# Kernel optimization log

Hardware: AMD Instinct MI355X
Metric: run time of the kernel (lower is better)

## Reference

```python
import jax, jax.numpy as jnp
import numpy as np

N_NODES = 100000
N_EDGES = 1600000
NEG_SLOPE = 0.2  # PyG GATConv default


def setup_inputs() -> dict:
    key = jax.random.key(0)
    ks = jax.random.split(key, 10)
    return {
        "x": jax.random.normal(ks[0], (N_NODES, 128), dtype=jnp.float32),
        "edge_index": jax.random.randint(ks[1], (2, N_EDGES), 0, N_NODES, dtype=jnp.int64),
        "W1": jax.random.normal(ks[2], (128, 128), dtype=jnp.float32) * 0.1,
        "a_src1": jax.random.normal(ks[3], (4, 32), dtype=jnp.float32) * 0.1,
        "a_dst1": jax.random.normal(ks[4], (4, 32), dtype=jnp.float32) * 0.1,
        "b1": jax.random.normal(ks[5], (128,), dtype=jnp.float32) * 0.1,
        "W2": jax.random.normal(ks[6], (128, 16), dtype=jnp.float32) * 0.1,
        "a_src2": jax.random.normal(ks[7], (1, 16), dtype=jnp.float32) * 0.1,
        "a_dst2": jax.random.normal(ks[8], (1, 16), dtype=jnp.float32) * 0.1,
        "b2": jax.random.normal(ks[9], (16,), dtype=jnp.float32) * 0.1,
    }


def _gat_layer(x, src, dst, W, a_src, a_dst, b, heads):
    # PyG GATConv (concat=True): xw -> per-edge attention -> segment softmax over
    # incoming edges of each target node -> weighted scatter-sum.
    N = x.shape[0]
    H = heads
    C = W.shape[1] // H
    xw = (x @ W).reshape(N, H, C)                      # [N,H,C]
    al = (xw * a_src).sum(-1)                          # [N,H] source term
    ar = (xw * a_dst).sum(-1)                          # [N,H] target term
    e = jax.nn.leaky_relu(al[src] + ar[dst], NEG_SLOPE)  # [E',H]
    emax = jax.ops.segment_max(e, dst, num_segments=N)   # [N,H]
    em = jnp.exp(e - emax[dst])
    denom = jax.ops.segment_sum(em, dst, num_segments=N)
    alpha = em / denom[dst]                            # [E',H]
    out = jax.ops.segment_sum(xw[src] * alpha[:, :, None], dst, num_segments=N)
    return out.reshape(N, H * C) + b


def reference(x, edge_index, W1, a_src1, a_dst1, b1, W2, a_src2, a_dst2, b2):
    N = x.shape[0]
    loop = jnp.arange(N, dtype=edge_index.dtype)
    # PyG GATConv add_self_loops=True
    src = jnp.concatenate([edge_index[0], loop])
    dst = jnp.concatenate([edge_index[1], loop])
    h = jax.nn.relu(_gat_layer(x, src, dst, W1, a_src1, a_dst1, b1, 4))
    # F.dropout(p=0.5, training=self.training): identity in eval mode
    return _gat_layer(h, src, dst, W2, a_src2, a_dst2, b2, 1)
```

## Files before the change

kernel.cpp:

```cpp
#include <hip/hip_runtime.h>
#include <hip/hip_fp16.h>

#define N_NODES 100000
#define N_EDGES 1600000
#define E_TOT   (N_EDGES + N_NODES)
#define NEG_SLOPE 0.2f
#define PART_EPB 4096
#define BSTRIDE 18432
#define NGEMM ((N_NODES + 63) / 64)
#define NPART ((E_TOT + PART_EPB - 1) / PART_EPB)

using f16x8 = __attribute__((ext_vector_type(8))) _Float16;
using f32x4 = __attribute__((ext_vector_type(4))) float;
union H8 { f16x8 v; _Float16 h[8]; __half2 h2[4]; };
union H4 { __half2 h2[2]; uint2 u; };

__global__ __launch_bounds__(256)
void k_gemm1_part(const float* __restrict__ x, const float* __restrict__ W1,
                  const float* __restrict__ a_src1, const float* __restrict__ a_dst1,
                  const int* __restrict__ ei, int* __restrict__ bcnt, int* __restrict__ pairs,
                  __half* __restrict__ xw1h, float* __restrict__ al1, float* __restrict__ ar1) {
    __shared__ int lcnt[128];
    __shared__ int lbase[128];
    __shared__ _Float16 sx[64][136];
    const int t = threadIdx.x;

    if (blockIdx.x >= NGEMM) {
        const int base = ((int)blockIdx.x - NGEMM) * PART_EPB;
        if (t < 128) lcnt[t] = 0;
        __syncthreads();
        int sr[16], dr[16];
#pragma unroll
        for (int u = 0; u < 16; ++u) {
            const int e = base + u * 256 + t;
            if (e < E_TOT) {
                int s, d;
                if (e < N_EDGES) { s = ei[e]; d = ei[N_EDGES + e]; }
                else             { s = d = e - N_EDGES; }
                sr[u] = s; dr[u] = d;
                atomicAdd(&lcnt[d >> 10], 1);
            } else dr[u] = -1;
        }
        __syncthreads();
        if (t < 128) {
            const int c = lcnt[t];
            lbase[t] = (c > 0) ? atomicAdd(&bcnt[t], c) : 0;
            lcnt[t] = 0;
        }
        __syncthreads();
#pragma unroll
        for (int u = 0; u < 16; ++u) {
            if (dr[u] >= 0) {
                const int bk = dr[u] >> 10;
                const int r = atomicAdd(&lcnt[bk], 1);
                pairs[(size_t)bk * BSTRIDE + lbase[bk] + r] = (sr[u] << 10) | (dr[u] & 1023);
            }
        }
        return;
    }

    const int n0 = (int)blockIdx.x * 64;

    for (int i = t; i < 64 * 32; i += 256) {
        const int row = i >> 5;
        const int c4 = (i & 31) * 4;
        const int gr = n0 + row;
        const float4 xv = *(const float4*)&x[(size_t)(gr < N_NODES ? gr : N_NODES - 1) * 128 + c4];
        H4 tmp;
        tmp.h2[0] = __float22half2_rn(make_float2(xv.x, xv.y));
        tmp.h2[1] = __float22half2_rn(make_float2(xv.z, xv.w));
        *(uint2*)&sx[row][c4] = tmp.u;
    }
    __syncthreads();

    const int lane = t & 63;
    const int w = t >> 6;
    const int q = lane >> 4;
    const int n15 = lane & 15;
    const int j0 = (2 * w) * 16 + n15;
    const int j1 = (2 * w + 1) * 16 + n15;

    f32x4 acc[4][2] = {};

    for (int kt = 0; kt < 4; ++kt) {
        const int k0 = kt * 32 + q * 8;
        H8 A0, A1, A2, A3, B0, B1;
        A0.v = *(const f16x8*)&sx[n15][k0];
        A1.v = *(const f16x8*)&sx[16 + n15][k0];
        A2.v = *(const f16x8*)&sx[32 + n15][k0];
        A3.v = *(const f16x8*)&sx[48 + n15][k0];
        {
            float w0[8], w1[8];
#pragma unroll
            for (int i = 0; i < 8; ++i) {
                w0[i] = W1[(size_t)(k0 + i) * 128 + j0];
                w1[i] = W1[(size_t)(k0 + i) * 128 + j1];
            }
#pragma unroll
            for (int i = 0; i < 4; ++i) {
                B0.h2[i] = __float22half2_rn(make_float2(w0[2 * i], w0[2 * i + 1]));
                B1.h2[i] = __float22half2_rn(make_float2(w1[2 * i], w1[2 * i + 1]));
            }
        }
        acc[0][0] = __builtin_amdgcn_mfma_f32_16x16x32_f16(A0.v, B0.v, acc[0][0], 0, 0, 0);
        acc[0][1] = __builtin_amdgcn_mfma_f32_16x16x32_f16(A0.v, B1.v, acc[0][1], 0, 0, 0);
        acc[1][0] = __builtin_amdgcn_mfma_f32_16x16x32_f16(A1.v, B0.v, acc[1][0], 0, 0, 0);
        acc[1][1] = __builtin_amdgcn_mfma_f32_16x16x32_f16(A1.v, B1.v, acc[1][1], 0, 0, 0);
        acc[2][0] = __builtin_amdgcn_mfma_f32_16x16x32_f16(A2.v, B0.v, acc[2][0], 0, 0, 0);
        acc[2][1] = __builtin_amdgcn_mfma_f32_16x16x32_f16(A2.v, B1.v, acc[2][1], 0, 0, 0);
        acc[3][0] = __builtin_amdgcn_mfma_f32_16x16x32_f16(A3.v, B0.v, acc[3][0], 0, 0, 0);
        acc[3][1] = __builtin_amdgcn_mfma_f32_16x16x32_f16(A3.v, B1.v, acc[3][1], 0, 0, 0);
    }

    const float as0 = a_src1[j0], as1 = a_src1[j1];
    const float ad0 = a_dst1[j0], ad1 = a_dst1[j1];
#pragma unroll
    for (int m = 0; m < 4; ++m) {
#pragma unroll
        for (int r = 0; r < 4; ++r) {
            const int node = n0 + m * 16 + q * 4 + r;
            const float vA = acc[m][0][r], vB = acc[m][1][r];
            const bool ok = node < N_NODES;
            if (ok) {
                xw1h[(size_t)node * 128 + j0] = __float2half(vA);
                xw1h[(size_t)node * 128 + j1] = __float2half(vB);
            }
            float ps = vA * as0 + vB * as1;
            float pd = vA * ad0 + vB * ad1;
#pragma unroll
            for (int o = 1; o < 16; o <<= 1) {
                ps += __shfl_xor(ps, o, 64);
                pd += __shfl_xor(pd, o, 64);
            }
            if (n15 == 0 && ok) {
                al1[(size_t)node * 4 + w] = ps;
                ar1[(size_t)node * 4 + w] = pd;
            }
        }
    }
}

__global__ __launch_bounds__(1024)
void k_fill3(const int* __restrict__ pairs, const int* __restrict__ bcnt,
             int* __restrict__ ioff, int* __restrict__ deg, int* __restrict__ ssrc) {
    const int bucket = blockIdx.x;
    const int t = threadIdx.x;
    const int cnt = bcnt[bucket];
    __shared__ int lhist[1024];
    __shared__ int lcur[1024];
    __shared__ int wsum[16];
    __shared__ int sbc[128];
    __shared__ int sbase;
    lhist[t] = 0;
    if (t < 128) sbc[t] = bcnt[t];
    __syncthreads();
    if (t == 0) {
        int b = 0;
        for (int k = 0; k < bucket; ++k) b += sbc[k];
        sbase = b;
    }
    for (int i = t; i < cnt; i += 1024) {
        const int p = pairs[(size_t)bucket * BSTRIDE + i];
        atomicAdd(&lhist[p & 1023], 1);
    }
    __syncthreads();
    const int v = lhist[t];
    int inc = v;
    const int lane = t & 63, wid = t >> 6;
#pragma unroll
    for (int o = 1; o < 64; o <<= 1) {
        const int nv = __shfl_up(inc, o, 64);
        if (lane >= o) inc += nv;
    }
    if (lane == 63) wsum[wid] = inc;
    __syncthreads();
    if (t == 0) {
        int acc = 0;
#pragma unroll
        for (int k = 0; k < 16; ++k) { const int tv = wsum[k]; wsum[k] = acc; acc += tv; }
    }
    __syncthreads();
    const int gofs = sbase + (inc - v) + wsum[wid];
    const int d = bucket * 1024 + t;
    if (d < N_NODES) { ioff[d] = gofs; deg[d] = v; }
    lcur[t] = gofs;
    __syncthreads();
    for (int i = t; i < cnt; i += 1024) {
        const int p = pairs[(size_t)bucket * BSTRIDE + i];
        const int pos = atomicAdd(&lcur[p & 1023], 1);
        ssrc[pos] = p >> 10;
    }
}

__global__ __launch_bounds__(256)
void k_aggr1(const int* __restrict__ ssrc, const int* __restrict__ offs,
             const int* __restrict__ deg, const float* __restrict__ al1,
             const float* __restrict__ ar1, const __half* __restrict__ xw1h,
             const float* __restrict__ b1, __half* __restrict__ out1h) {
    const int lane = threadIdx.x & 63;
    const int d = blockIdx.x * 4 + (threadIdx.x >> 6);
    const int g = lane >> 4;
    const int c = lane & 15;
    const int h = c >> 2;
    const int beg = offs[d];
    const int n = deg[d];
    const float arh = ar1[(size_t)d * 4 + h];
    float acc[8] = {0.f, 0.f, 0.f, 0.f, 0.f, 0.f, 0.f, 0.f};
    float dnm = 0.f;

    for (int base = 0; base < n; base += 8) {
#pragma unroll
        for (int u = 0; u < 2; ++u) {
            const int e = base + u * 4 + g;
            const bool p = e < n;
            const int s = ssrc[beg + (p ? e : 0)];
            float v = al1[(size_t)s * 4 + h] + arh;
            v = v > 0.f ? v : NEG_SLOPE * v;
            const float w = p ? __expf(v) : 0.f;
            const uint4 rv = *(const uint4*)&xw1h[(size_t)s * 128 + c * 8];
            const float2 f0 = __half22float2(*(const __half2*)&rv.x);
            const float2 f1 = __half22float2(*(const __half2*)&rv.y);
            const float2 f2 = __half22float2(*(const __half2*)&rv.z);
            const float2 f3 = __half22float2(*(const __half2*)&rv.w);
            acc[0] = fmaf(w, f0.x, acc[0]); acc[1] = fmaf(w, f0.y, acc[1]);
            acc[2] = fmaf(w, f1.x, acc[2]); acc[3] = fmaf(w, f1.y, acc[3]);
            acc[4] = fmaf(w, f2.x, acc[4]); acc[5] = fmaf(w, f2.y, acc[5]);
            acc[6] = fmaf(w, f3.x, acc[6]); acc[7] = fmaf(w, f3.y, acc[7]);
            dnm += w;
        }
    }
#pragma unroll
    for (int i = 0; i < 8; ++i) {
        acc[i] += __shfl_xor(acc[i], 16, 64);
        acc[i] += __shfl_xor(acc[i], 32, 64);
    }
    dnm += __shfl_xor(dnm, 16, 64);
    dnm += __shfl_xor(dnm, 32, 64);
    if (g == 0) {
        const float rc = 1.f / dnm;
        const float4 b01 = *(const float4*)&b1[c * 8];
        const float4 b23 = *(const float4*)&b1[c * 8 + 4];
        const float bb[8] = {b01.x, b01.y, b01.z, b01.w, b23.x, b23.y, b23.z, b23.w};
        __half ho[8];
#pragma unroll
        for (int i = 0; i < 8; ++i) {
            const float hv = acc[i] * rc + bb[i];
            ho[i] = __float2half(hv > 0.f ? hv : 0.f);
        }
        *(uint4*)&out1h[(size_t)d * 128 + c * 8] = *(uint4*)ho;
    }
}

__global__ __launch_bounds__(256)
void k_gemm2m(const __half* __restrict__ out1h, const float* __restrict__ W2,
              const float* __restrict__ a_src2, const float* __restrict__ a_dst2,
              __half* __restrict__ xw2h, float* __restrict__ al2, float* __restrict__ ar2) {
    const int t = threadIdx.x;
    const int lane = t & 63;
    const int w = t >> 6;
    const int q = lane >> 4;
    const int n15 = lane & 15;
    const int n0 = (int)blockIdx.x * 128 + w * 16;
    const int ra0 = n0 + n15;
    const int ra1 = n0 + 64 + n15;
    const size_t rowA0 = (ra0 < N_NODES) ? (size_t)ra0 : (size_t)(N_NODES - 1);
    const size_t rowA1 = (ra1 < N_NODES) ? (size_t)ra1 : (size_t)(N_NODES - 1);

    f32x4 acc0 = {0.f, 0.f, 0.f, 0.f}, acc1 = acc0;
#pragma unroll
    for (int kt = 0; kt < 4; ++kt) {
        const int k0 = kt * 32 + q * 8;
        H8 A0, A1, B;
        A0.v = *(const f16x8*)&out1h[rowA0 * 128 + k0];
        A1.v = *(const f16x8*)&out1h[rowA1 * 128 + k0];
        float wv[8];
#pragma unroll
        for (int i = 0; i < 8; ++i)
            wv[i] = W2[(size_t)(k0 + i) * 16 + n15];
#pragma unroll
        for (int i = 0; i < 4; ++i)
            B.h2[i] = __float22half2_rn(make_float2(wv[2 * i], wv[2 * i + 1]));
        acc0 = __builtin_amdgcn_mfma_f32_16x16x32_f16(A0.v, B.v, acc0, 0, 0, 0);
        acc1 = __builtin_amdgcn_mfma_f32_16x16x32_f16(A1.v, B.v, acc1, 0, 0, 0);
    }

    const float as = a_src2[n15], ad = a_dst2[n15];
#pragma unroll
    for (int m = 0; m < 2; ++m) {
        const f32x4 acc = m ? acc1 : acc0;
#pragma unroll
        for (int r = 0; r < 4; ++r) {
            const int node = n0 + m * 64 + q * 4 + r;
            float ps = acc[r] * as;
            float pd = acc[r] * ad;
#pragma unroll
            for (int o = 1; o < 16; o <<= 1) {
                ps += __shfl_xor(ps, o, 64);
                pd += __shfl_xor(pd, o, 64);
            }
            if (node < N_NODES) {
                xw2h[(size_t)node * 16 + n15] = __float2half(acc[r]);
                if (n15 == 0) { al2[node] = ps; ar2[node] = pd; }
            }
        }
    }
}

__global__ __launch_bounds__(256)
void k_aggr2(const int* __restrict__ ssrc, const int* __restrict__ offs,
             const int* __restrict__ deg, const float* __restrict__ al2,
             const float* __restrict__ ar2, const __half* __restrict__ xw2h,
             const float* __restrict__ b2, float* __restrict__ out) {
    const int lane = threadIdx.x & 63;
    const int node = blockIdx.x * 4 + (threadIdx.x >> 6);
    const int j2 = lane & 7;
    const int eL = lane >> 3;
    const int beg = offs[node];
    const int n = deg[node];
    const float ard = ar2[node];
    float a0 = 0.f, a1 = 0.f, dnm = 0.f;
    for (int base = 0; base < n; base += 32) {
#pragma unroll
        for (int u = 0; u < 4; ++u) {
            const int e = base + u * 8 + eL;
            const bool p = e < n;
            const int s = ssrc[beg + (p ? e : 0)];
            float v = al2[s] + ard;
            v = v > 0.f ? v : NEG_SLOPE * v;
            const float w = p ? __expf(v) : 0.f;
            const float2 f = __half22float2(*(const __half2*)&xw2h[(size_t)s * 16 + j2 * 2]);
            a0 = fmaf(w, f.x, a0);
            a1 = fmaf(w, f.y, a1);
            dnm += w;
        }
    }
#pragma unroll
    for (int o = 8; o < 64; o <<= 1) {
        a0 += __shfl_xor(a0, o, 64);
        a1 += __shfl_xor(a1, o, 64);
        dnm += __shfl_xor(dnm, o, 64);
    }
    if (eL == 0) {
        out[(size_t)node * 16 + j2 * 2]     = a0 / dnm + b2[j2 * 2];
        out[(size_t)node * 16 + j2 * 2 + 1] = a1 / dnm + b2[j2 * 2 + 1];
    }
}

extern "C" void kernel_launch(void* const* d_in, const int* in_sizes, int n_in,
                              void* d_out, int out_size, void* d_ws, size_t ws_size,
                              hipStream_t stream) {
    const float* x      = (const float*)d_in[0];
    const int*   ei     = (const int*)d_in[1];
    const float* W1     = (const float*)d_in[2];
    const float* a_src1 = (const float*)d_in[3];
    const float* a_dst1 = (const float*)d_in[4];
    const float* b1     = (const float*)d_in[5];
    const float* W2     = (const float*)d_in[6];
    const float* a_src2 = (const float*)d_in[7];
    const float* a_dst2 = (const float*)d_in[8];
    const float* b2     = (const float*)d_in[9];
    float* out = (float*)d_out;

    char* wsb = (char*)d_ws;
    __half* xw1h = (__half*)wsb;
    __half* xw2h = (__half*)wsb;
    float*  al2  = (float*)(wsb + (size_t)N_NODES * 16 * 2);
    float*  ar2  = al2 + N_NODES;
    __half* out1h = (__half*)(wsb + (size_t)N_NODES * 128 * 2);
    int*    pairs = (int*)out1h;
    float*  al1  = (float*)(wsb + (size_t)N_NODES * 128 * 4);
    float*  ar1  = al1 + (size_t)N_NODES * 4;
    int* ibcnt = (int*)(ar1 + (size_t)N_NODES * 4);
    int* ioff  = ibcnt + 128;
    int* ideg  = ioff + N_NODES;
    int* isrc  = ideg + N_NODES;

    hipMemsetAsync(ibcnt, 0, 128 * sizeof(int), stream);

    k_gemm1_part<<<NGEMM + NPART, 256, 0, stream>>>(x, W1, a_src1, a_dst1,
                                                    ei, ibcnt, pairs, xw1h, al1, ar1);
    k_fill3<<<128, 1024, 0, stream>>>(pairs, ibcnt, ioff, ideg, isrc);

    k_aggr1<<<N_NODES / 4, 256, 0, stream>>>(isrc, ioff, ideg, al1, ar1, xw1h, b1, out1h);

    k_gemm2m<<<(N_NODES + 127) / 128, 256, 0, stream>>>(out1h, W2, a_src2, a_dst2, xw2h, al2, ar2);

    k_aggr2<<<N_NODES / 4, 256, 0, stream>>>(isrc, ioff, ideg, al2, ar2, xw2h, b2, out);
}
```

Measured before the change: 298.7 us.

## Fold attention vectors into weights and use finer destination buckets for CSR build

Adds a prep kernel that precomputes W·a_src and W·a_dst as fp16 matrices so the attention logits come from extra MFMA ops instead of shuffle reductions in both GEMM kernels; the prep kernel also zeroes the bucket counters, replacing the memset. Destination bucketing in the edge partition and fill kernels changes from 1024-node to 256-node buckets (391 blocks of 256 threads instead of 128 blocks of 1024), giving more parallelism in the CSR build. Logits now pass through an fp16-rounded fused weight, which slightly changes numerics, and one extra tiny launch is added.

```diff
diff --git a/kernel.cpp b/kernel.cpp
--- a/kernel.cpp
+++ b/kernel.cpp
@@ -6,7 +6,8 @@
 #define E_TOT   (N_EDGES + N_NODES)
 #define NEG_SLOPE 0.2f
 #define PART_EPB 4096
-#define BSTRIDE 18432
+#define NBUCK ((N_NODES + 255) / 256)
+#define PBSTRIDE 5632
 #define NGEMM ((N_NODES + 63) / 64)
 #define NPART ((E_TOT + PART_EPB - 1) / PART_EPB)
 
@@ -15,19 +16,66 @@
 union H8 { f16x8 v; _Float16 h[8]; __half2 h2[4]; };
 union H4 { __half2 h2[2]; uint2 u; };
 
+__global__ __launch_bounds__(128)
+void k_prep(const float* __restrict__ W1, const float* __restrict__ as1,
+            const float* __restrict__ ad1, const float* __restrict__ W2,
+            const float* __restrict__ as2, const float* __restrict__ ad2,
+            _Float16* __restrict__ WaT1, _Float16* __restrict__ WaT2,
+            int* __restrict__ bcnt) {
+    const int t = threadIdx.x;
+    for (int i = t; i < NBUCK; i += 128) bcnt[i] = 0;
+
+    const float a1s = as1[t], a1d = ad1[t];
+    for (int k = 0; k < 128; ++k) {
+        const float wv = W1[(size_t)k * 128 + t];
+        float ps = wv * a1s;
+        float pd = wv * a1d;
+#pragma unroll
+        for (int o = 1; o < 32; o <<= 1) {
+            ps += __shfl_xor(ps, o, 32);
+            pd += __shfl_xor(pd, o, 32);
+        }
+        if ((t & 31) == 0) {
+            const int h = t >> 5;
+            WaT1[h * 128 + k] = (_Float16)ps;
+            WaT1[(4 + h) * 128 + k] = (_Float16)pd;
+        }
+    }
+    for (int n = 8; n < 16; ++n) WaT1[n * 128 + t] = (_Float16)0.f;
+
+    const int j = t & 15, kb = t >> 4;
+    const float a2s = as2[j], a2d = ad2[j];
+    for (int k8 = 0; k8 < 16; ++k8) {
+        const int k = k8 * 8 + kb;
+        const float wv = W2[(size_t)k * 16 + j];
+        float ps = wv * a2s;
+        float pd = wv * a2d;
+#pragma unroll
+        for (int o = 1; o < 16; o <<= 1) {
+            ps += __shfl_xor(ps, o, 16);
+            pd += __shfl_xor(pd, o, 16);
+        }
+        if (j == 0) {
+            WaT2[k] = (_Float16)ps;
+            WaT2[128 + k] = (_Float16)pd;
+        }
+    }
+    for (int n = 2; n < 16; ++n) WaT2[n * 128 + t] = (_Float16)0.f;
+}
+
 __global__ __launch_bounds__(256)
 void k_gemm1_part(const float* __restrict__ x, const float* __restrict__ W1,
-                  const float* __restrict__ a_src1, const float* __restrict__ a_dst1,
+                  const _Float16* __restrict__ WaT1,
                   const int* __restrict__ ei, int* __restrict__ bcnt, int* __restrict__ pairs,
                   __half* __restrict__ xw1h, float* __restrict__ al1, float* __restrict__ ar1) {
-    __shared__ int lcnt[128];
-    __shared__ int lbase[128];
+    __shared__ int lcnt[NBUCK + 1];
+    __shared__ int lbase[NBUCK + 1];
     __shared__ _Float16 sx[64][136];
     const int t = threadIdx.x;
 
     if (blockIdx.x >= NGEMM) {
         const int base = ((int)blockIdx.x - NGEMM) * PART_EPB;
-        if (t < 128) lcnt[t] = 0;
+        for (int i = t; i < NBUCK; i += 256) lcnt[i] = 0;
         __syncthreads();
         int sr[16], dr[16];
 #pragma unroll
@@ -38,22 +86,22 @@
                 if (e < N_EDGES) { s = ei[e]; d = ei[N_EDGES + e]; }
                 else             { s = d = e - N_EDGES; }
                 sr[u] = s; dr[u] = d;
-                atomicAdd(&lcnt[d >> 10], 1);
+                atomicAdd(&lcnt[d >> 8], 1);
             } else dr[u] = -1;
         }
         __syncthreads();
-        if (t < 128) {
-            const int c = lcnt[t];
-            lbase[t] = (c > 0) ? atomicAdd(&bcnt[t], c) : 0;
-            lcnt[t] = 0;
+        for (int i = t; i < NBUCK; i += 256) {
+            const int c = lcnt[i];
+            lbase[i] = (c > 0) ? atomicAdd(&bcnt[i], c) : 0;
+            lcnt[i] = 0;
         }
         __syncthreads();
 #pragma unroll
         for (int u = 0; u < 16; ++u) {
             if (dr[u] >= 0) {
-                const int bk = dr[u] >> 10;
+                const int bk = dr[u] >> 8;
                 const int r = atomicAdd(&lcnt[bk], 1);
-                pairs[(size_t)bk * BSTRIDE + lbase[bk] + r] = (sr[u] << 10) | (dr[u] & 1023);
+                pairs[(size_t)bk * PBSTRIDE + lbase[bk] + r] = (sr[u] << 8) | (dr[u] & 255);
             }
         }
         return;
@@ -81,6 +129,7 @@
     const int j1 = (2 * w + 1) * 16 + n15;
 
     f32x4 acc[4][2] = {};
+    f32x4 e0 = {0.f,0.f,0.f,0.f}, e1 = e0, e2 = e0, e3 = e0;
 
     for (int kt = 0; kt < 4; ++kt) {
         const int k0 = kt * 32 + q * 8;
@@ -110,58 +159,65 @@
         acc[2][1] = __builtin_amdgcn_mfma_f32_16x16x32_f16(A2.v, B1.v, acc[2][1], 0, 0, 0);
         acc[3][0] = __builtin_amdgcn_mfma_f32_16x16x32_f16(A3.v, B0.v, acc[3][0], 0, 0, 0);
         acc[3][1] = __builtin_amdgcn_mfma_f32_16x16x32_f16(A3.v, B1.v, acc[3][1], 0, 0, 0);
-    }
-
-    const float as0 = a_src1[j0], as1 = a_src1[j1];
-    const float ad0 = a_dst1[j0], ad1 = a_dst1[j1];
+        if (w == 0) {
+            H8 B2;
+            B2.v = *(const f16x8*)&WaT1[n15 * 128 + k0];
+            e0 = __builtin_amdgcn_mfma_f32_16x16x32_f16(A0.v, B2.v, e0, 0, 0, 0);
+            e1 = __builtin_amdgcn_mfma_f32_16x16x32_f16(A1.v, B2.v, e1, 0, 0, 0);
+            e2 = __builtin_amdgcn_mfma_f32_16x16x32_f16(A2.v, B2.v, e2, 0, 0, 0);
+            e3 = __builtin_amdgcn_mfma_f32_16x16x32_f16(A3.v, B2.v, e3, 0, 0, 0);
+        }
+    }
+
 #pragma unroll
     for (int m = 0; m < 4; ++m) {
 #pragma unroll
         for (int r = 0; r < 4; ++r) {
             const int node = n0 + m * 16 + q * 4 + r;
-            const float vA = acc[m][0][r], vB = acc[m][1][r];
-            const bool ok = node < N_NODES;
-            if (ok) {
-                xw1h[(size_t)node * 128 + j0] = __float2half(vA);
-                xw1h[(size_t)node * 128 + j1] = __float2half(vB);
-            }
-            float ps = vA * as0 + vB * as1;
-            float pd = vA * ad0 + vB * ad1;
-#pragma unroll
-            for (int o = 1; o < 16; o <<= 1) {
-                ps += __shfl_xor(ps, o, 64);
-                pd += __shfl_xor(pd, o, 64);
-            }
-            if (n15 == 0 && ok) {
-                al1[(size_t)node * 4 + w] = ps;
-                ar1[(size_t)node * 4 + w] = pd;
-            }
-        }
-    }
-}
-
-__global__ __launch_bounds__(1024)
+            if (node < N_NODES) {
+                xw1h[(size_t)node * 128 + j0] = __float2half(acc[m][0][r]);
+                xw1h[(size_t)node * 128 + j1] = __float2half(acc[m][1][r]);
+            }
+        }
+    }
+    if (w == 0) {
+#pragma unroll
+        for (int m = 0; m < 4; ++m) {
+            const f32x4 em = (m == 0) ? e0 : (m == 1) ? e1 : (m == 2) ? e2 : e3;
+#pragma unroll
+            for (int r = 0; r < 4; ++r) {
+                const int node = n0 + m * 16 + q * 4 + r;
+                if (node < N_NODES) {
+                    if (n15 < 4)      al1[(size_t)node * 4 + n15] = em[r];
+                    else if (n15 < 8) ar1[(size_t)node * 4 + (n15 - 4)] = em[r];
+                }
+            }
+        }
+    }
+}
+
+__global__ __launch_bounds__(256)
 void k_fill3(const int* __restrict__ pairs, const int* __restrict__ bcnt,
              int* __restrict__ ioff, int* __restrict__ deg, int* __restrict__ ssrc) {
     const int bucket = blockIdx.x;
     const int t = threadIdx.x;
     const int cnt = bcnt[bucket];
-    __shared__ int lhist[1024];
-    __shared__ int lcur[1024];
-    __shared__ int wsum[16];
-    __shared__ int sbc[128];
+    __shared__ int lhist[256];
+    __shared__ int lcur[256];
+    __shared__ int wsum[4];
+    __shared__ int sbc[NBUCK + 1];
     __shared__ int sbase;
     lhist[t] = 0;
-    if (t < 128) sbc[t] = bcnt[t];
+    for (int i = t; i < NBUCK; i += 256) sbc[i] = bcnt[i];
     __syncthreads();
     if (t == 0) {
         int b = 0;
         for (int k = 0; k < bucket; ++k) b += sbc[k];
         sbase = b;
     }
-    for (int i = t; i < cnt; i += 1024) {
-        const int p = pairs[(size_t)bucket * BSTRIDE + i];
-        atomicAdd(&lhist[p & 1023], 1);
+    for (int i = t; i < cnt; i += 256) {
+        const int p = pairs[(size_t)bucket * PBSTRIDE + i];
+        atomicAdd(&lhist[p & 255], 1);
     }
     __syncthreads();
     const int v = lhist[t];
@@ -177,18 +233,18 @@
     if (t == 0) {
         int acc = 0;
 #pragma unroll
-        for (int k = 0; k < 16; ++k) { const int tv = wsum[k]; wsum[k] = acc; acc += tv; }
+        for (int k = 0; k < 4; ++k) { const int tv = wsum[k]; wsum[k] = acc; acc += tv; }
     }
     __syncthreads();
     const int gofs = sbase + (inc - v) + wsum[wid];
-    const int d = bucket * 1024 + t;
+    const int d = bucket * 256 + t;
     if (d < N_NODES) { ioff[d] = gofs; deg[d] = v; }
     lcur[t] = gofs;
     __syncthreads();
-    for (int i = t; i < cnt; i += 1024) {
-        const int p = pairs[(size_t)bucket * BSTRIDE + i];
-        const int pos = atomicAdd(&lcur[p & 1023], 1);
-        ssrc[pos] = p >> 10;
+    for (int i = t; i < cnt; i += 256) {
+        const int p = pairs[(size_t)bucket * PBSTRIDE + i];
+        const int pos = atomicAdd(&lcur[p & 255], 1);
+        ssrc[pos] = p >> 8;
     }
 }
 
@@ -253,7 +309,7 @@
 
 __global__ __launch_bounds__(256)
 void k_gemm2m(const __half* __restrict__ out1h, const float* __restrict__ W2,
-              const float* __restrict__ a_src2, const float* __restrict__ a_dst2,
+              const _Float16* __restrict__ WaT2,
               __half* __restrict__ xw2h, float* __restrict__ al2, float* __restrict__ ar2) {
     const int t = threadIdx.x;
     const int lane = t & 63;
@@ -267,10 +323,11 @@
     const size_t rowA1 = (ra1 < N_NODES) ? (size_t)ra1 : (size_t)(N_NODES - 1);
 
     f32x4 acc0 = {0.f, 0.f, 0.f, 0.f}, acc1 = acc0;
+    f32x4 e0 = acc0, e1 = acc0;
 #pragma unroll
     for (int kt = 0; kt < 4; ++kt) {
         const int k0 = kt * 32 + q * 8;
-        H8 A0, A1, B;
+        H8 A0, A1, B, B2;
         A0.v = *(const f16x8*)&out1h[rowA0 * 128 + k0];
         A1.v = *(const f16x8*)&out1h[rowA1 * 128 + k0];
         float wv[8];
@@ -280,27 +337,24 @@
 #pragma unroll
         for (int i = 0; i < 4; ++i)
             B.h2[i] = __float22half2_rn(make_float2(wv[2 * i], wv[2 * i + 1]));
+        B2.v = *(const f16x8*)&WaT2[n15 * 128 + k0];
         acc0 = __builtin_amdgcn_mfma_f32_16x16x32_f16(A0.v, B.v, acc0, 0, 0, 0);
         acc1 = __builtin_amdgcn_mfma_f32_16x16x32_f16(A1.v, B.v, acc1, 0, 0, 0);
-    }
-
-    const float as = a_src2[n15], ad = a_dst2[n15];
+        e0   = __builtin_amdgcn_mfma_f32_16x16x32_f16(A0.v, B2.v, e0, 0, 0, 0);
+        e1   = __builtin_amdgcn_mfma_f32_16x16x32_f16(A1.v, B2.v, e1, 0, 0, 0);
+    }
+
 #pragma unroll
     for (int m = 0; m < 2; ++m) {
         const f32x4 acc = m ? acc1 : acc0;
+        const f32x4 em  = m ? e1 : e0;
 #pragma unroll
         for (int r = 0; r < 4; ++r) {
             const int node = n0 + m * 64 + q * 4 + r;
-            float ps = acc[r] * as;
-            float pd = acc[r] * ad;
-#pragma unroll
-            for (int o = 1; o < 16; o <<= 1) {
-                ps += __shfl_xor(ps, o, 64);
-                pd += __shfl_xor(pd, o, 64);
-            }
             if (node < N_NODES) {
                 xw2h[(size_t)node * 16 + n15] = __float2half(acc[r]);
-                if (n15 == 0) { al2[node] = ps; ar2[node] = pd; }
+                if (n15 == 0)      al2[node] = em[r];
+                else if (n15 == 1) ar2[node] = em[r];
             }
         }
     }
@@ -371,19 +425,22 @@
     float*  al1  = (float*)(wsb + (size_t)N_NODES * 128 * 4);
     float*  ar1  = al1 + (size_t)N_NODES * 4;
     int* ibcnt = (int*)(ar1 + (size_t)N_NODES * 4);
-    int* ioff  = ibcnt + 128;
+    int* ioff  = ibcnt + 512;
     int* ideg  = ioff + N_NODES;
     int* isrc  = ideg + N_NODES;
-
-    hipMemsetAsync(ibcnt, 0, 128 * sizeof(int), stream);
-
-    k_gemm1_part<<<NGEMM + NPART, 256, 0, stream>>>(x, W1, a_src1, a_dst1,
-                                                    ei, ibcnt, pairs, xw1h, al1, ar1);
-    k_fill3<<<128, 1024, 0, stream>>>(pairs, ibcnt, ioff, ideg, isrc);
+    _Float16* WaT1 = (_Float16*)(isrc + E_TOT);
+    _Float16* WaT2 = WaT1 + 16 * 128;
+
+    k_prep<<<1, 128, 0, stream>>>(W1, a_src1, a_dst1, W2, a_src2, a_dst2,
+                                  WaT1, WaT2, ibcnt);
+
+    k_gemm1_part<<<NGEMM + NPART, 256, 0, stream>>>(x, W1, WaT1, ei, ibcnt,
+                                                    pairs, xw1h, al1, ar1);
+    k_fill3<<<NBUCK, 256, 0, stream>>>(pairs, ibcnt, ioff, ideg, isrc);
 
     k_aggr1<<<N_NODES / 4, 256, 0, stream>>>(isrc, ioff, ideg, al1, ar1, xw1h, b1, out1h);
 
-    k_gemm2m<<<(N_NODES + 127) / 128, 256, 0, stream>>>(out1h, W2, a_src2, a_dst2, xw2h, al2, ar2);
+    k_gemm2m<<<(N_NODES + 127) / 128, 256, 0, stream>>>(out1h, W2, WaT2, xw2h, al2, ar2);
 
     k_aggr2<<<N_NODES / 4, 256, 0, stream>>>(isrc, ioff, ideg, al2, ar2, xw2h, b2, out);
 }
```

Measured after the change: 350.8 us. +17.4%, slower.

## Co-schedule CSR fill with GEMM1 instead of partition pass

Applied to the files above, without the earlier changes.

The edge-partition pass now runs as its own kernel. The per-bucket CSR fill runs in the same launch as the first-layer GEMM, with the fill blocks first and using 256 threads each over a shared-memory union. The intent is to hide the 128 latency-bound fill blocks behind the GEMM blocks rather than behind the partition work. The cost is that the fill uses 256 instead of 1024 threads per bucket, so each fill block does more serial work, and the shared-memory union sizes every block to the larger of the two layouts.

```diff
diff --git a/kernel.cpp b/kernel.cpp
--- a/kernel.cpp
+++ b/kernel.cpp
@@ -9,57 +9,120 @@
 #define BSTRIDE 18432
 #define NGEMM ((N_NODES + 63) / 64)
 #define NPART ((E_TOT + PART_EPB - 1) / PART_EPB)
+#define NFILL 128
 
 using f16x8 = __attribute__((ext_vector_type(8))) _Float16;
 using f32x4 = __attribute__((ext_vector_type(4))) float;
 union H8 { f16x8 v; _Float16 h[8]; __half2 h2[4]; };
 union H4 { __half2 h2[2]; uint2 u; };
 
+
 __global__ __launch_bounds__(256)
-void k_gemm1_part(const float* __restrict__ x, const float* __restrict__ W1,
-                  const float* __restrict__ a_src1, const float* __restrict__ a_dst1,
-                  const int* __restrict__ ei, int* __restrict__ bcnt, int* __restrict__ pairs,
-                  __half* __restrict__ xw1h, float* __restrict__ al1, float* __restrict__ ar1) {
+void k_part(const int* __restrict__ ei, int* __restrict__ bcnt, int* __restrict__ pairs) {
     __shared__ int lcnt[128];
     __shared__ int lbase[128];
-    __shared__ _Float16 sx[64][136];
     const int t = threadIdx.x;
-
-    if (blockIdx.x >= NGEMM) {
-        const int base = ((int)blockIdx.x - NGEMM) * PART_EPB;
-        if (t < 128) lcnt[t] = 0;
+    const int base = (int)blockIdx.x * PART_EPB;
+    if (t < 128) lcnt[t] = 0;
+    __syncthreads();
+    int sr[16], dr[16];
+#pragma unroll
+    for (int u = 0; u < 16; ++u) {
+        const int e = base + u * 256 + t;
+        if (e < E_TOT) {
+            int s, d;
+            if (e < N_EDGES) { s = ei[e]; d = ei[N_EDGES + e]; }
+            else             { s = d = e - N_EDGES; }
+            sr[u] = s; dr[u] = d;
+            atomicAdd(&lcnt[d >> 10], 1);
+        } else dr[u] = -1;
+    }
+    __syncthreads();
+    if (t < 128) {
+        const int c = lcnt[t];
+        lbase[t] = (c > 0) ? atomicAdd(&bcnt[t], c) : 0;
+        lcnt[t] = 0;
+    }
+    __syncthreads();
+#pragma unroll
+    for (int u = 0; u < 16; ++u) {
+        if (dr[u] >= 0) {
+            const int bk = dr[u] >> 10;
+            const int r = atomicAdd(&lcnt[bk], 1);
+            pairs[(size_t)bk * BSTRIDE + lbase[bk] + r] = (sr[u] << 10) | (dr[u] & 1023);
+        }
+    }
+}
+
+union SMem {
+    _Float16 sx[64][136];
+    struct { int lhist[1024]; int lcur[1024]; int sbc[128]; int wsum[4]; int sbase; } f;
+};
+
+__global__ __launch_bounds__(256)
+void k_gemm1_fill(const float* __restrict__ x, const float* __restrict__ W1,
+                  const float* __restrict__ a_src1, const float* __restrict__ a_dst1,
+                  const int* __restrict__ bcnt, const int* __restrict__ pairs,
+                  int* __restrict__ ioff, int* __restrict__ deg, int* __restrict__ ssrc,
+                  __half* __restrict__ xw1h, float* __restrict__ al1, float* __restrict__ ar1) {
+    __shared__ SMem sm;
+    const int t = threadIdx.x;
+
+    if (blockIdx.x < NFILL) {
+        const int bucket = blockIdx.x;
+        const int cnt = bcnt[bucket];
+        auto& F = sm.f;
+        for (int i = t; i < 1024; i += 256) F.lhist[i] = 0;
+        if (t < 128) F.sbc[t] = bcnt[t];
         __syncthreads();
-        int sr[16], dr[16];
-#pragma unroll
-        for (int u = 0; u < 16; ++u) {
-            const int e = base + u * 256 + t;
-            if (e < E_TOT) {
-                int s, d;
-                if (e < N_EDGES) { s = ei[e]; d = ei[N_EDGES + e]; }
-                else             { s = d = e - N_EDGES; }
-                sr[u] = s; dr[u] = d;
-                atomicAdd(&lcnt[d >> 10], 1);
-            } else dr[u] = -1;
+        if (t == 0) {
+            int b = 0;
+            for (int k = 0; k < bucket; ++k) b += F.sbc[k];
+            F.sbase = b;
+        }
+        for (int i = t; i < cnt; i += 256) {
+            const int p = pairs[(size_t)bucket * BSTRIDE + i];
+            atomicAdd(&F.lhist[p & 1023], 1);
         }
         __syncthreads();
-        if (t < 128) {
-            const int c = lcnt[t];
-            lbase[t] = (c > 0) ? atomicAdd(&bcnt[t], c) : 0;
-            lcnt[t] = 0;
-        }
+        const int h0 = F.lhist[4 * t], h1 = F.lhist[4 * t + 1];
+        const int h2 = F.lhist[4 * t + 2], h3 = F.lhist[4 * t + 3];
+        const int sum = h0 + h1 + h2 + h3;
+        int inc = sum;
+        const int lane = t & 63, wid = t >> 6;
+#pragma unroll
+        for (int o = 1; o < 64; o <<= 1) {
+            const int nv = __shfl_up(inc, o, 64);
+            if (lane >= o) inc += nv;
+        }
+        if (lane == 63) F.wsum[wid] = inc;
         __syncthreads();
-#pragma unroll
-        for (int u = 0; u < 16; ++u) {
-            if (dr[u] >= 0) {
-                const int bk = dr[u] >> 10;
-                const int r = atomicAdd(&lcnt[bk], 1);
-                pairs[(size_t)bk * BSTRIDE + lbase[bk] + r] = (sr[u] << 10) | (dr[u] & 1023);
-            }
+        if (t == 0) {
+            int acc = 0;
+#pragma unroll
+            for (int k = 0; k < 4; ++k) { const int tv = F.wsum[k]; F.wsum[k] = acc; acc += tv; }
+        }
+        __syncthreads();
+        const int base = F.sbase + (inc - sum) + F.wsum[wid];
+        const int pp[4] = {base, base + h0, base + h0 + h1, base + h0 + h1 + h2};
+        const int hh[4] = {h0, h1, h2, h3};
+        const int d0 = (bucket << 10) + 4 * t;
+#pragma unroll
+        for (int i = 0; i < 4; ++i) {
+            const int d = d0 + i;
+            if (d < N_NODES) { ioff[d] = pp[i]; deg[d] = hh[i]; }
+            F.lcur[4 * t + i] = pp[i];
+        }
+        __syncthreads();
+        for (int i = t; i < cnt; i += 256) {
+            const int p = pairs[(size_t)bucket * BSTRIDE + i];
+            const int pos = atomicAdd(&F.lcur[p & 1023], 1);
+            ssrc[pos] = p >> 10;
         }
         return;
     }
 
-    const int n0 = (int)blockIdx.x * 64;
+    const int n0 = ((int)blockIdx.x - NFILL) * 64;
 
     for (int i = t; i < 64 * 32; i += 256) {
         const int row = i >> 5;
@@ -69,7 +132,7 @@
         H4 tmp;
         tmp.h2[0] = __float22half2_rn(make_float2(xv.x, xv.y));
         tmp.h2[1] = __float22half2_rn(make_float2(xv.z, xv.w));
-        *(uint2*)&sx[row][c4] = tmp.u;
+        *(uint2*)&sm.sx[row][c4] = tmp.u;
     }
     __syncthreads();
 
@@ -85,10 +148,10 @@
     for (int kt = 0; kt < 4; ++kt) {
         const int k0 = kt * 32 + q * 8;
         H8 A0, A1, A2, A3, B0, B1;
-        A0.v = *(const f16x8*)&sx[n15][k0];
-        A1.v = *(const f16x8*)&sx[16 + n15][k0];
-        A2.v = *(const f16x8*)&sx[32 + n15][k0];
-        A3.v = *(const f16x8*)&sx[48 + n15][k0];
+        A0.v = *(const f16x8*)&sm.sx[n15][k0];
+        A1.v = *(const f16x8*)&sm.sx[16 + n15][k0];
+        A2.v = *(const f16x8*)&sm.sx[32 + n15][k0];
+        A3.v = *(const f16x8*)&sm.sx[48 + n15][k0];
         {
             float w0[8], w1[8];
 #pragma unroll
@@ -137,58 +200,6 @@
                 ar1[(size_t)node * 4 + w] = pd;
             }
         }
-    }
-}
-
-__global__ __launch_bounds__(1024)
-void k_fill3(const int* __restrict__ pairs, const int* __restrict__ bcnt,
-             int* __restrict__ ioff, int* __restrict__ deg, int* __restrict__ ssrc) {
-    const int bucket = blockIdx.x;
-    const int t = threadIdx.x;
-    const int cnt = bcnt[bucket];
-    __shared__ int lhist[1024];
-    __shared__ int lcur[1024];
-    __shared__ int wsum[16];
-    __shared__ int sbc[128];
-    __shared__ int sbase;
-    lhist[t] = 0;
-    if (t < 128) sbc[t] = bcnt[t];
-    __syncthreads();
-    if (t == 0) {
-        int b = 0;
-        for (int k = 0; k < bucket; ++k) b += sbc[k];
-        sbase = b;
-    }
-    for (int i = t; i < cnt; i += 1024) {
-        const int p = pairs[(size_t)bucket * BSTRIDE + i];
-        atomicAdd(&lhist[p & 1023], 1);
-    }
-    __syncthreads();
-    const int v = lhist[t];
-    int inc = v;
-    const int lane = t & 63, wid = t >> 6;
-#pragma unroll
-    for (int o = 1; o < 64; o <<= 1) {
-        const int nv = __shfl_up(inc, o, 64);
-        if (lane >= o) inc += nv;
-    }
-    if (lane == 63) wsum[wid] = inc;
-    __syncthreads();
-    if (t == 0) {
-        int acc = 0;
-#pragma unroll
-        for (int k = 0; k < 16; ++k) { const int tv = wsum[k]; wsum[k] = acc; acc += tv; }
-    }
-    __syncthreads();
-    const int gofs = sbase + (inc - v) + wsum[wid];
-    const int d = bucket * 1024 + t;
-    if (d < N_NODES) { ioff[d] = gofs; deg[d] = v; }
-    lcur[t] = gofs;
-    __syncthreads();
-    for (int i = t; i < cnt; i += 1024) {
-        const int p = pairs[(size_t)bucket * BSTRIDE + i];
-        const int pos = atomicAdd(&lcur[p & 1023], 1);
-        ssrc[pos] = p >> 10;
     }
 }
 
@@ -377,9 +388,11 @@
 
     hipMemsetAsync(ibcnt, 0, 128 * sizeof(int), stream);
 
-    k_gemm1_part<<<NGEMM + NPART, 256, 0, stream>>>(x, W1, a_src1, a_dst1,
-                                                    ei, ibcnt, pairs, xw1h, al1, ar1);
-    k_fill3<<<128, 1024, 0, stream>>>(pairs, ibcnt, ioff, ideg, isrc);
+    k_part<<<NPART, 256, 0, stream>>>(ei, ibcnt, pairs);
+
+    k_gemm1_fill<<<NFILL + NGEMM, 256, 0, stream>>>(x, W1, a_src1, a_dst1,
+                                                    ibcnt, pairs, ioff, ideg, isrc,
+                                                    xw1h, al1, ar1);
 
     k_aggr1<<<N_NODES / 4, 256, 0, stream>>>(isrc, ioff, ideg, al1, ar1, xw1h, b1, out1h);
 
```

Result: slower. 312.6 us (+4.7%).
